# Kernel optimization log

Measured on AMD Instinct MI355X. Metric: run time of the kernel, lower is better.

Reference implementation:

```python
import jax, jax.numpy as jnp
import numpy as np

N_QUBITS = 8
NUM_HEADS = 2
N_QLAYERS = 1
B, S = 8, 2048


def _apply_rx(state, theta, wire, n):
    # state: (N, 2**n) complex64; theta: scalar or (N,) rotation angle on `wire`
    st = state.reshape(-1, 2 ** wire, 2, 2 ** (n - wire - 1))
    theta = jnp.asarray(theta, jnp.float32)
    c = jnp.cos(0.5 * theta)
    s = jnp.sin(0.5 * theta)
    if theta.ndim == 1:
        c = c[:, None, None]
        s = s[:, None, None]
    js = 1j * s  # complex64 via weak promotion
    a0 = st[:, :, 0, :]
    a1 = st[:, :, 1, :]
    b0 = c * a0 - js * a1
    b1 = -js * a0 + c * a1
    return jnp.stack([b0, b1], axis=2).reshape(-1, 2 ** n)


def _apply_cnot(state, ctrl, tgt, n):
    s = state.reshape((-1,) + (2,) * n)
    s0 = jnp.take(s, 0, axis=1 + ctrl)
    s1 = jnp.take(s, 1, axis=1 + ctrl)
    t_ax = 1 + tgt - (1 if tgt > ctrl else 0)  # target axis after removing ctrl axis
    s1 = jnp.flip(s1, axis=t_ax)  # X on target when ctrl == 1
    return jnp.stack([s0, s1], axis=1 + ctrl).reshape(-1, 2 ** n)


def _circuit(x, w, n):
    # PennyLane ansatz 1: AngleEmbedding (RX) + BasicEntanglerLayers (RX + ring CNOTs),
    # then <Z_i> for every wire. x: (N, n) angles, w: (L, n) trainable angles.
    N = x.shape[0]
    state = jnp.zeros((N, 2 ** n), jnp.complex64).at[:, 0].set(1.0)
    for i in range(n):  # AngleEmbedding, rotation='X'
        state = _apply_rx(state, x[:, i], i, n)
    for l in range(w.shape[0]):  # BasicEntanglerLayers
        for i in range(n):
            state = _apply_rx(state, w[l, i], i, n)
        for i in range(n):  # ring entangler
            state = _apply_cnot(state, i, (i + 1) % n, n)
    probs = jnp.real(state * jnp.conj(state)).reshape((-1,) + (2,) * n)
    zs = [jnp.sum(jnp.take(probs, 0, axis=1 + i) - jnp.take(probs, 1, axis=1 + i),
                  axis=tuple(range(1, n))) for i in range(n)]
    return jnp.stack(zs, axis=-1)  # (N, n)


def setup_inputs() -> dict:
    key = jax.random.key(0)
    ks = jax.random.split(key, 8)
    q = jax.random.normal(ks[0], (B, S, N_QUBITS), jnp.float32)
    k = jax.random.normal(ks[1], (B, S, N_QUBITS), jnp.float32)
    v = jax.random.normal(ks[2], (B, S, N_QUBITS), jnp.float32)
    # additive causal mask (1 where attention is disallowed)
    mask = (1.0 - jnp.tril(jnp.ones((S, S), jnp.float32)))[None, None, :, :]
    two_pi = 2.0 * np.pi
    Wq = jax.random.uniform(ks[3], (N_QLAYERS, N_QUBITS), jnp.float32, 0.0, two_pi)
    Wk = jax.random.uniform(ks[4], (N_QLAYERS, N_QUBITS), jnp.float32, 0.0, two_pi)
    Wv = jax.random.uniform(ks[5], (N_QLAYERS, N_QUBITS), jnp.float32, 0.0, two_pi)
    Wd = jax.random.uniform(ks[6], (N_QLAYERS, N_QUBITS), jnp.float32, 0.0, two_pi)
    return {"v": v, "k": k, "q": q, "mask": mask, "Wq": Wq, "Wk": Wk, "Wv": Wv, "Wd": Wd}


def reference(v, k, q, mask, Wq, Wk, Wv, Wd):
    Bq, Sq, E = q.shape
    n = E
    H = NUM_HEADS
    d = E // H

    def proj(x, W):  # batched PQC over all B*S tokens (replaces per-timestep loop)
        return _circuit(x.reshape(-1, n), W, n).reshape(x.shape)

    qp = proj(q, Wq)
    kp = proj(k, Wk)
    vp = proj(v, Wv)

    def heads(x):  # (B, S, E) -> (B, H, S, d)
        return x.reshape(Bq, -1, H, d).transpose(0, 2, 1, 3)

    qh, kh, vh = heads(qp), heads(kp), heads(vp)
    logits = jnp.einsum('bhqd,bhkd->bhqk', qh, kh) / jnp.sqrt(jnp.float32(d))
    logits = logits + mask * (-1e9)
    attn = jax.nn.softmax(logits, axis=-1)
    ctx = jnp.einsum('bhqk,bhkd->bhqd', attn, vh)
    concat = ctx.transpose(0, 2, 1, 3).reshape(Bq, -1, E)
    out = proj(concat, Wd)
    return out, attn
```

## Files before the change

### kernel.cpp

```cpp
#include <hip/hip_runtime.h>
#include <math.h>

namespace {

constexpr int SEQ   = 2048;
constexpr int BAT   = 8;
constexpr int NHEAD = 2;

__device__ __forceinline__ void qproj8(const float th[8], float z[8]) {
    float c[8];
#pragma unroll
    for (int i = 0; i < 8; ++i) c[i] = __cosf(th[i]);
    z[1] = c[0] * c[1];
#pragma unroll
    for (int i = 2; i < 8; ++i) z[i] = z[i - 1] * c[i];
    float p = c[1] * c[2];
    p *= c[3] * c[4];
    p *= c[5] * c[6];
    p *= c[7];
    z[0] = p;
}

__global__ __launch_bounds__(512, 4) void attn_kernel(
    const float* __restrict__ vin, const float* __restrict__ kin,
    const float* __restrict__ qin,
    const float* __restrict__ Wq, const float* __restrict__ Wk,
    const float* __restrict__ Wv,
    float* __restrict__ ctx_out,
    float* __restrict__ attn)
{
    __shared__ float4 Ksh[SEQ];
    __shared__ float4 Vsh[SEQ];

    const int bb  = blockIdx.x;
    const int bh  = bb >> 5;
    const int blk = bb & 31;
    const int b   = bh >> 1;
    const int h   = bh & 1;
    const int hc  = h * 4;

    float wk[8], wv[8];
#pragma unroll
    for (int i = 0; i < 8; ++i) { wk[i] = Wk[i]; wv[i] = Wv[i]; }

    for (int r = threadIdx.x; r < SEQ; r += 512) {
        const float4* k4 = reinterpret_cast<const float4*>(kin + ((size_t)b * SEQ + r) * 8);
        float4 ka = k4[0], kb = k4[1];
        float th[8], z[8];
        th[0] = ka.x + wk[0]; th[1] = ka.y + wk[1]; th[2] = ka.z + wk[2]; th[3] = ka.w + wk[3];
        th[4] = kb.x + wk[4]; th[5] = kb.y + wk[5]; th[6] = kb.z + wk[6]; th[7] = kb.w + wk[7];
        qproj8(th, z);
        Ksh[r] = make_float4(z[hc], z[hc + 1], z[hc + 2], z[hc + 3]);

        const float4* v4 = reinterpret_cast<const float4*>(vin + ((size_t)b * SEQ + r) * 8);
        float4 va = v4[0], vb = v4[1];
        th[0] = va.x + wv[0]; th[1] = va.y + wv[1]; th[2] = va.z + wv[2]; th[3] = va.w + wv[3];
        th[4] = vb.x + wv[4]; th[5] = vb.y + wv[5]; th[6] = vb.z + wv[6]; th[7] = vb.w + wv[7];
        qproj8(th, z);
        Vsh[r] = make_float4(z[hc], z[hc + 1], z[hc + 2], z[hc + 3]);
    }
    __syncthreads();

    const int wave = threadIdx.x >> 6;
    const int lane = threadIdx.x & 63;

    float wq[8];
#pragma unroll
    for (int i = 0; i < 8; ++i) wq[i] = Wq[i];

    for (int it = 0; it < 8; ++it) {
        const int qrow = blk + 32 * (it * 8 + wave);

        const float4* q4 = reinterpret_cast<const float4*>(qin + ((size_t)b * SEQ + qrow) * 8);
        float4 qa = q4[0], qb = q4[1];
        float th[8], z[8];
        th[0] = qa.x + wq[0]; th[1] = qa.y + wq[1]; th[2] = qa.z + wq[2]; th[3] = qa.w + wq[3];
        th[4] = qb.x + wq[4]; th[5] = qb.y + wq[5]; th[6] = qb.z + wq[6]; th[7] = qb.w + wq[7];
        qproj8(th, z);
        const float qf0 = z[hc], qf1 = z[hc + 1], qf2 = z[hc + 2], qf3 = z[hc + 3];

        const int nc4 = (qrow >> 8) + 1;
        float pr[8][4];
        float s = 0.f, cx = 0.f, cy = 0.f, cz = 0.f, cw = 0.f;
#pragma unroll
        for (int c = 0; c < 8; ++c) {
            if (c < nc4) {
                const int k0 = c * 256 + lane * 4;
                float4 K0 = Ksh[k0], K1 = Ksh[k0 + 1], K2 = Ksh[k0 + 2], K3 = Ksh[k0 + 3];
                float4 V0 = Vsh[k0], V1 = Vsh[k0 + 1], V2 = Vsh[k0 + 2], V3 = Vsh[k0 + 3];
                float l0 = 0.5f * (qf0 * K0.x + qf1 * K0.y + qf2 * K0.z + qf3 * K0.w);
                float l1 = 0.5f * (qf0 * K1.x + qf1 * K1.y + qf2 * K1.z + qf3 * K1.w);
                float l2 = 0.5f * (qf0 * K2.x + qf1 * K2.y + qf2 * K2.z + qf3 * K2.w);
                float l3 = 0.5f * (qf0 * K3.x + qf1 * K3.y + qf2 * K3.z + qf3 * K3.w);
                float p0 = (k0 + 0 <= qrow) ? __expf(l0 - 2.0f) : 0.0f;
                float p1 = (k0 + 1 <= qrow) ? __expf(l1 - 2.0f) : 0.0f;
                float p2 = (k0 + 2 <= qrow) ? __expf(l2 - 2.0f) : 0.0f;
                float p3 = (k0 + 3 <= qrow) ? __expf(l3 - 2.0f) : 0.0f;
                pr[c][0] = p0; pr[c][1] = p1; pr[c][2] = p2; pr[c][3] = p3;
                s += p0 + p1 + p2 + p3;
                cx += p0 * V0.x + p1 * V1.x + p2 * V2.x + p3 * V3.x;
                cy += p0 * V0.y + p1 * V1.y + p2 * V2.y + p3 * V3.y;
                cz += p0 * V0.z + p1 * V1.z + p2 * V2.z + p3 * V3.z;
                cw += p0 * V0.w + p1 * V1.w + p2 * V2.w + p3 * V3.w;
            }
        }
#pragma unroll
        for (int off = 32; off >= 1; off >>= 1) {
            s  += __shfl_xor(s,  off, 64);
            cx += __shfl_xor(cx, off, 64);
            cy += __shfl_xor(cy, off, 64);
            cz += __shfl_xor(cz, off, 64);
            cw += __shfl_xor(cw, off, 64);
        }
        const float inv = 1.0f / s;

        float4* arow4 = reinterpret_cast<float4*>(attn + (((size_t)bh * SEQ) + qrow) * SEQ);
#pragma unroll
        for (int c = 0; c < 8; ++c) {
            float4 o = (c < nc4)
                ? make_float4(pr[c][0] * inv, pr[c][1] * inv, pr[c][2] * inv, pr[c][3] * inv)
                : make_float4(0.f, 0.f, 0.f, 0.f);
            arow4[c * 64 + lane] = o;
        }

        if (lane == 0) {
            float4* o = reinterpret_cast<float4*>(ctx_out + ((size_t)b * SEQ + qrow) * 8 + hc);
            *o = make_float4(cx * inv, cy * inv, cz * inv, cw * inv);
        }
    }
}

__global__ __launch_bounds__(256) void finalize_kernel(
    float* __restrict__ ctx, const float* __restrict__ Wd)
{
    const int r = blockIdx.x * 256 + threadIdx.x;
    if (r >= BAT * SEQ) return;
    float4* p4 = reinterpret_cast<float4*>(ctx + (size_t)r * 8);
    float4 a = p4[0], c = p4[1];
    float th[8], z[8];
    th[0] = a.x + Wd[0]; th[1] = a.y + Wd[1]; th[2] = a.z + Wd[2]; th[3] = a.w + Wd[3];
    th[4] = c.x + Wd[4]; th[5] = c.y + Wd[5]; th[6] = c.z + Wd[6]; th[7] = c.w + Wd[7];
    qproj8(th, z);
    p4[0] = make_float4(z[0], z[1], z[2], z[3]);
    p4[1] = make_float4(z[4], z[5], z[6], z[7]);
}

}

extern "C" void kernel_launch(void* const* d_in, const int* in_sizes, int n_in,
                              void* d_out, int out_size, void* d_ws, size_t ws_size,
                              hipStream_t stream) {
    const float* v  = (const float*)d_in[0];
    const float* k  = (const float*)d_in[1];
    const float* q  = (const float*)d_in[2];
    const float* Wq = (const float*)d_in[4];
    const float* Wk = (const float*)d_in[5];
    const float* Wv = (const float*)d_in[6];
    const float* Wd = (const float*)d_in[7];

    float* out  = (float*)d_out;
    float* attn = out + (size_t)BAT * SEQ * 8;

    hipLaunchKernelGGL(attn_kernel, dim3(BAT * NHEAD * 32), dim3(512), 0, stream,
                       v, k, q, Wq, Wk, Wv, out, attn);
    hipLaunchKernelGGL(finalize_kernel, dim3((BAT * SEQ) / 256), dim3(256), 0, stream,
                       out, Wd);
}
```

Before: 59.28 us.

## Store K/V projections as half in LDS, double grid, restructure attention stores

K and V projections are kept in shared memory as fp16, halving LDS use so more blocks can be resident (launch bounds raised to 8). The grid doubles to 64 blocks per batch-head, with each block handling 32 query rows instead of 64. Zero chunks of the attention row are written first, and probabilities are kept as packed halves in registers and stored as scalar coalesced writes with a strided key mapping. The fp16 rounding of K, V and the unnormalized probabilities lowers the precision of the attention outputs and context.

```diff
diff --git a/kernel.cpp b/kernel.cpp
--- a/kernel.cpp
+++ b/kernel.cpp
@@ -1,11 +1,14 @@
 #include <hip/hip_runtime.h>
+#include <hip/hip_fp16.h>
 #include <math.h>
 
 namespace {
 
-constexpr int SEQ   = 2048;
-constexpr int BAT   = 8;
-constexpr int NHEAD = 2;
+constexpr int SEQ = 2048;
+constexpr int BAT = 8;
+
+struct alignas(8) h4 { __half2 lo, hi; };
+typedef float f4 __attribute__((ext_vector_type(4)));
 
 __device__ __forceinline__ void qproj8(const float th[8], float z[8]) {
     float c[8];
@@ -21,7 +24,7 @@
     z[0] = p;
 }
 
-__global__ __launch_bounds__(512, 4) void attn_kernel(
+__global__ __launch_bounds__(512, 8) void attn_kernel(
     const float* __restrict__ vin, const float* __restrict__ kin,
     const float* __restrict__ qin,
     const float* __restrict__ Wq, const float* __restrict__ Wk,
@@ -29,103 +32,115 @@
     float* __restrict__ ctx_out,
     float* __restrict__ attn)
 {
-    __shared__ float4 Ksh[SEQ];
-    __shared__ float4 Vsh[SEQ];
+    __shared__ h4 Ksh[SEQ];
+    __shared__ h4 Vsh[SEQ];
 
     const int bb  = blockIdx.x;
-    const int bh  = bb >> 5;
-    const int blk = bb & 31;
+    const int bh  = bb >> 6;
+    const int g   = bb & 63;
     const int b   = bh >> 1;
     const int h   = bh & 1;
     const int hc  = h * 4;
+    const int tid  = threadIdx.x;
+    const int wave = tid >> 6;
+    const int lane = tid & 63;
 
-    float wk[8], wv[8];
-#pragma unroll
-    for (int i = 0; i < 8; ++i) { wk[i] = Wk[i]; wv[i] = Wv[i]; }
-
-    for (int r = threadIdx.x; r < SEQ; r += 512) {
+    for (int r = tid; r < SEQ; r += 512) {
         const float4* k4 = reinterpret_cast<const float4*>(kin + ((size_t)b * SEQ + r) * 8);
         float4 ka = k4[0], kb = k4[1];
         float th[8], z[8];
-        th[0] = ka.x + wk[0]; th[1] = ka.y + wk[1]; th[2] = ka.z + wk[2]; th[3] = ka.w + wk[3];
-        th[4] = kb.x + wk[4]; th[5] = kb.y + wk[5]; th[6] = kb.z + wk[6]; th[7] = kb.w + wk[7];
+        th[0] = ka.x + Wk[0]; th[1] = ka.y + Wk[1]; th[2] = ka.z + Wk[2]; th[3] = ka.w + Wk[3];
+        th[4] = kb.x + Wk[4]; th[5] = kb.y + Wk[5]; th[6] = kb.z + Wk[6]; th[7] = kb.w + Wk[7];
         qproj8(th, z);
-        Ksh[r] = make_float4(z[hc], z[hc + 1], z[hc + 2], z[hc + 3]);
+        h4 t;
+        t.lo = __floats2half2_rn(z[hc + 0], z[hc + 1]);
+        t.hi = __floats2half2_rn(z[hc + 2], z[hc + 3]);
+        Ksh[r] = t;
 
         const float4* v4 = reinterpret_cast<const float4*>(vin + ((size_t)b * SEQ + r) * 8);
         float4 va = v4[0], vb = v4[1];
-        th[0] = va.x + wv[0]; th[1] = va.y + wv[1]; th[2] = va.z + wv[2]; th[3] = va.w + wv[3];
-        th[4] = vb.x + wv[4]; th[5] = vb.y + wv[5]; th[6] = vb.z + wv[6]; th[7] = vb.w + wv[7];
+        th[0] = va.x + Wv[0]; th[1] = va.y + Wv[1]; th[2] = va.z + Wv[2]; th[3] = va.w + Wv[3];
+        th[4] = vb.x + Wv[4]; th[5] = vb.y + Wv[5]; th[6] = vb.z + Wv[6]; th[7] = vb.w + Wv[7];
         qproj8(th, z);
-        Vsh[r] = make_float4(z[hc], z[hc + 1], z[hc + 2], z[hc + 3]);
+        t.lo = __floats2half2_rn(z[hc + 0], z[hc + 1]);
+        t.hi = __floats2half2_rn(z[hc + 2], z[hc + 3]);
+        Vsh[r] = t;
     }
     __syncthreads();
 
-    const int wave = threadIdx.x >> 6;
-    const int lane = threadIdx.x & 63;
+    for (int it = 0; it < 4; ++it) {
+        const int qrow = g + 64 * (it * 8 + wave);
+        float* arow = attn + ((size_t)bh * SEQ + qrow) * SEQ;
+        const int nc = (qrow >> 8) + 1;
 
-    float wq[8];
-#pragma unroll
-    for (int i = 0; i < 8; ++i) wq[i] = Wq[i];
-
-    for (int it = 0; it < 8; ++it) {
-        const int qrow = blk + 32 * (it * 8 + wave);
+        f4* arow4 = reinterpret_cast<f4*>(arow);
+        const f4 zz = {0.f, 0.f, 0.f, 0.f};
+        for (int c = nc; c < 8; ++c)
+            arow4[c * 64 + lane] = zz;
 
         const float4* q4 = reinterpret_cast<const float4*>(qin + ((size_t)b * SEQ + qrow) * 8);
         float4 qa = q4[0], qb = q4[1];
         float th[8], z[8];
-        th[0] = qa.x + wq[0]; th[1] = qa.y + wq[1]; th[2] = qa.z + wq[2]; th[3] = qa.w + wq[3];
-        th[4] = qb.x + wq[4]; th[5] = qb.y + wq[5]; th[6] = qb.z + wq[6]; th[7] = qb.w + wq[7];
+        th[0] = qa.x + Wq[0]; th[1] = qa.y + Wq[1]; th[2] = qa.z + Wq[2]; th[3] = qa.w + Wq[3];
+        th[4] = qb.x + Wq[4]; th[5] = qb.y + Wq[5]; th[6] = qb.z + Wq[6]; th[7] = qb.w + Wq[7];
         qproj8(th, z);
-        const float qf0 = z[hc], qf1 = z[hc + 1], qf2 = z[hc + 2], qf3 = z[hc + 3];
+        const float q0 = 0.5f * z[hc + 0], q1 = 0.5f * z[hc + 1];
+        const float q2 = 0.5f * z[hc + 2], q3 = 0.5f * z[hc + 3];
 
-        const int nc4 = (qrow >> 8) + 1;
-        float pr[8][4];
-        float s = 0.f, cx = 0.f, cy = 0.f, cz = 0.f, cw = 0.f;
+        __half2 pk[8][2];
+        float s = 0.f, c0 = 0.f, c1 = 0.f, c2 = 0.f, c3 = 0.f;
 #pragma unroll
         for (int c = 0; c < 8; ++c) {
-            if (c < nc4) {
-                const int k0 = c * 256 + lane * 4;
-                float4 K0 = Ksh[k0], K1 = Ksh[k0 + 1], K2 = Ksh[k0 + 2], K3 = Ksh[k0 + 3];
-                float4 V0 = Vsh[k0], V1 = Vsh[k0 + 1], V2 = Vsh[k0 + 2], V3 = Vsh[k0 + 3];
-                float l0 = 0.5f * (qf0 * K0.x + qf1 * K0.y + qf2 * K0.z + qf3 * K0.w);
-                float l1 = 0.5f * (qf0 * K1.x + qf1 * K1.y + qf2 * K1.z + qf3 * K1.w);
-                float l2 = 0.5f * (qf0 * K2.x + qf1 * K2.y + qf2 * K2.z + qf3 * K2.w);
-                float l3 = 0.5f * (qf0 * K3.x + qf1 * K3.y + qf2 * K3.z + qf3 * K3.w);
-                float p0 = (k0 + 0 <= qrow) ? __expf(l0 - 2.0f) : 0.0f;
-                float p1 = (k0 + 1 <= qrow) ? __expf(l1 - 2.0f) : 0.0f;
-                float p2 = (k0 + 2 <= qrow) ? __expf(l2 - 2.0f) : 0.0f;
-                float p3 = (k0 + 3 <= qrow) ? __expf(l3 - 2.0f) : 0.0f;
-                pr[c][0] = p0; pr[c][1] = p1; pr[c][2] = p2; pr[c][3] = p3;
-                s += p0 + p1 + p2 + p3;
-                cx += p0 * V0.x + p1 * V1.x + p2 * V2.x + p3 * V3.x;
-                cy += p0 * V0.y + p1 * V1.y + p2 * V2.y + p3 * V3.y;
-                cz += p0 * V0.z + p1 * V1.z + p2 * V2.z + p3 * V3.z;
-                cw += p0 * V0.w + p1 * V1.w + p2 * V2.w + p3 * V3.w;
+            if (c < nc) {
+                float p[4];
+#pragma unroll
+                for (int i = 0; i < 4; ++i) {
+                    const int k = c * 256 + i * 64 + lane;
+                    h4 K = Ksh[k];
+                    h4 V = Vsh[k];
+                    float2 ka = __half22float2(K.lo), kb = __half22float2(K.hi);
+                    float l = fmaf(q0, ka.x, fmaf(q1, ka.y,
+                              fmaf(q2, kb.x, fmaf(q3, kb.y, -2.0f))));
+                    float pe = __expf(l);
+                    pe = (k <= qrow) ? pe : 0.0f;
+                    p[i] = pe;
+                    s += pe;
+                    float2 va = __half22float2(V.lo), vb = __half22float2(V.hi);
+                    c0 += pe * va.x; c1 += pe * va.y;
+                    c2 += pe * vb.x; c3 += pe * vb.y;
+                }
+                pk[c][0] = __floats2half2_rn(p[0], p[1]);
+                pk[c][1] = __floats2half2_rn(p[2], p[3]);
             }
         }
+
+#pragma unroll
+        for (int off = 32; off >= 1; off >>= 1)
+            s += __shfl_xor(s, off, 64);
+        const float inv = 1.0f / s;
+
+#pragma unroll
+        for (int c = 0; c < 8; ++c) {
+            if (c < nc) {
+                float2 pa = __half22float2(pk[c][0]);
+                float2 pb = __half22float2(pk[c][1]);
+                arow[c * 256 +   0 + lane] = pa.x * inv;
+                arow[c * 256 +  64 + lane] = pa.y * inv;
+                arow[c * 256 + 128 + lane] = pb.x * inv;
+                arow[c * 256 + 192 + lane] = pb.y * inv;
+            }
+        }
+
 #pragma unroll
         for (int off = 32; off >= 1; off >>= 1) {
-            s  += __shfl_xor(s,  off, 64);
-            cx += __shfl_xor(cx, off, 64);
-            cy += __shfl_xor(cy, off, 64);
-            cz += __shfl_xor(cz, off, 64);
-            cw += __shfl_xor(cw, off, 64);
+            c0 += __shfl_xor(c0, off, 64);
+            c1 += __shfl_xor(c1, off, 64);
+            c2 += __shfl_xor(c2, off, 64);
+            c3 += __shfl_xor(c3, off, 64);
         }
-        const float inv = 1.0f / s;
-
-        float4* arow4 = reinterpret_cast<float4*>(attn + (((size_t)bh * SEQ) + qrow) * SEQ);
-#pragma unroll
-        for (int c = 0; c < 8; ++c) {
-            float4 o = (c < nc4)
-                ? make_float4(pr[c][0] * inv, pr[c][1] * inv, pr[c][2] * inv, pr[c][3] * inv)
-                : make_float4(0.f, 0.f, 0.f, 0.f);
-            arow4[c * 64 + lane] = o;
-        }
-
         if (lane == 0) {
             float4* o = reinterpret_cast<float4*>(ctx_out + ((size_t)b * SEQ + qrow) * 8 + hc);
-            *o = make_float4(cx * inv, cy * inv, cz * inv, cw * inv);
+            *o = make_float4(c0 * inv, c1 * inv, c2 * inv, c3 * inv);
         }
     }
 }
@@ -161,7 +176,7 @@
     float* out  = (float*)d_out;
     float* attn = out + (size_t)BAT * SEQ * 8;
 
-    hipLaunchKernelGGL(attn_kernel, dim3(BAT * NHEAD * 32), dim3(512), 0, stream,
+    hipLaunchKernelGGL(attn_kernel, dim3(BAT * 2 * 64), dim3(512), 0, stream,
                        v, k, q, Wq, Wk, Wv, out, attn);
     hipLaunchKernelGGL(finalize_kernel, dim3((BAT * SEQ) / 256), dim3(256), 0, stream,
                        out, Wd);
```

New measurement: 130.6 us. 120% more time.
